# Optimization experiments

Hardware: AMD Instinct MI355X
Metric: run time of the kernel (lower is better)

Reference implementation:

```python
import math
import jax, jax.numpy as jnp
import numpy as np

NUM_HEADS = 16

def _alibi_slopes(n):
    def pow2(n):
        start = 2 ** (-2 ** (-(math.log2(n) - 3)))
        return [start * start ** i for i in range(n)]
    if math.log2(n).is_integer():
        return pow2(n)
    c = 2 ** math.floor(math.log2(n))
    return pow2(c) + _alibi_slopes(2 * c)[0::2][: n - c]

def _alibi_bias(num_heads, L):
    pos = np.arange(L)
    rel = (pos[None, :] - pos[:, None]).astype(np.float32)  # [L, L]
    slopes = np.asarray(_alibi_slopes(num_heads), dtype=np.float32)[:, None, None]
    bias = slopes * rel[None, :, :]  # [H, L, L]
    causal = pos[None, :] <= pos[:, None]
    bias = np.where(causal[None, :, :], bias, -np.inf).astype(np.float32)
    return jnp.asarray(bias)[None]  # [1, H, L, L]

def setup_inputs() -> dict:
    key = jax.random.key(0)
    ks = jax.random.split(key, 4)
    B, L, D = 2, 2048, 1024
    x = jax.random.normal(ks[0], (B, L, D), dtype=jnp.float32)
    W_in = jax.random.normal(ks[1], (D, 3 * D), dtype=jnp.float32) * 0.02
    b_in = jnp.zeros((3 * D,), dtype=jnp.float32)
    W_out = jax.random.normal(ks[2], (D, D), dtype=jnp.float32) * 0.02
    b_out = jnp.zeros((D,), dtype=jnp.float32)
    return {"x": x, "W_in": W_in, "b_in": b_in, "W_out": W_out, "b_out": b_out}

def reference(x, W_in, b_in, W_out, b_out):
    B, L, D = x.shape
    H = NUM_HEADS
    Dh = D // H
    qkv = x @ W_in + b_in  # [B, L, 3D]
    q, k, v = jnp.split(qkv, 3, axis=-1)
    # [B, H, L, Dh]
    q = q.reshape(B, L, H, Dh).transpose(0, 2, 1, 3)
    k = k.reshape(B, L, H, Dh).transpose(0, 2, 1, 3)
    v = v.reshape(B, L, H, Dh).transpose(0, 2, 1, 3)
    attn = jnp.einsum("bhqd,bhkd->bhqk", q, k) * (1.0 / math.sqrt(Dh))
    attn = attn + _alibi_bias(H, L)  # ALiBi + causal mask (-inf above diag)
    p = jax.nn.softmax(attn, axis=-1)
    out = jnp.einsum("bhqk,bhkd->bhqd", p, v)
    out = out.transpose(0, 2, 1, 3).reshape(B, L, D)
    out = out @ W_out + b_out
    return out, k, v
```

## Files before the change

### kernel.cpp

```cpp
#include <hip/hip_runtime.h>
#include <math.h>

typedef __bf16 bf16x8 __attribute__((ext_vector_type(8)));
typedef float  f32x4  __attribute__((ext_vector_type(4)));
typedef unsigned short u16x4 __attribute__((ext_vector_type(4)));

#define BATCH  2
#define SEQ    2048
#define DMODEL 1024
#define NHEAD  16
#define DHEAD  64
#define MROWS  4096
#define N_QKV  3072
#define KDIM   1024
#define OUTSECT (MROWS*DMODEL)

#define LOG2E 1.44269504088896f
#define QSCALE (0.125f * LOG2E)

__device__ inline __bf16 f2bf(float f) {
    unsigned u = __builtin_bit_cast(unsigned, f);
    unsigned r = (u + 0x7fffu + ((u >> 16) & 1u)) >> 16;
    return __builtin_bit_cast(__bf16, (unsigned short)r);
}

__device__ inline void gload16(const void* g, void* l) {
    __builtin_amdgcn_global_load_lds(
        (const __attribute__((address_space(1))) void*)g,
        (__attribute__((address_space(3))) void*)l, 16, 0, 0);
}

__device__ inline float dpp_max16(float x) {
    int v, t;
    v = __builtin_bit_cast(int, x);
    t = __builtin_amdgcn_update_dpp(v, v, 0xB1, 0xF, 0xF, false);
    x = fmaxf(x, __builtin_bit_cast(float, t));
    v = __builtin_bit_cast(int, x);
    t = __builtin_amdgcn_update_dpp(v, v, 0x4E, 0xF, 0xF, false);
    x = fmaxf(x, __builtin_bit_cast(float, t));
    v = __builtin_bit_cast(int, x);
    t = __builtin_amdgcn_update_dpp(v, v, 0x128, 0xF, 0xF, false);
    x = fmaxf(x, __builtin_bit_cast(float, t));
    v = __builtin_bit_cast(int, x);
    t = __builtin_amdgcn_update_dpp(v, v, 0x140, 0xF, 0xF, false);
    x = fmaxf(x, __builtin_bit_cast(float, t));
    return x;
}
__device__ inline float dpp_sum16(float x) {
    int v, t;
    v = __builtin_bit_cast(int, x);
    t = __builtin_amdgcn_update_dpp(v, v, 0xB1, 0xF, 0xF, false);
    x += __builtin_bit_cast(float, t);
    v = __builtin_bit_cast(int, x);
    t = __builtin_amdgcn_update_dpp(v, v, 0x4E, 0xF, 0xF, false);
    x += __builtin_bit_cast(float, t);
    v = __builtin_bit_cast(int, x);
    t = __builtin_amdgcn_update_dpp(v, v, 0x128, 0xF, 0xF, false);
    x += __builtin_bit_cast(float, t);
    v = __builtin_bit_cast(int, x);
    t = __builtin_amdgcn_update_dpp(v, v, 0x140, 0xF, 0xF, false);
    x += __builtin_bit_cast(float, t);
    return x;
}


__global__ __launch_bounds__(256) void cvt_x_k(const float* __restrict__ x,
                                               __bf16* __restrict__ xb) {
    size_t i = (size_t)blockIdx.x * 256 + threadIdx.x;
    const float4* p = (const float4*)x + i * 2;
    float4 a = p[0], b = p[1];
    __bf16 o[8] = {f2bf(a.x), f2bf(a.y), f2bf(a.z), f2bf(a.w),
                   f2bf(b.x), f2bf(b.y), f2bf(b.z), f2bf(b.w)};
    *(bf16x8*)(xb + i * 8) = *(bf16x8*)o;
}

__global__ __launch_bounds__(256) void cvt_wt_k(const float* __restrict__ W,
                                                __bf16* __restrict__ Wt, int Nw) {
    __shared__ float t[64][65];
    const int k0 = blockIdx.y * 64, n0 = blockIdx.x * 64;
    const int tid = threadIdx.x;
    #pragma unroll
    for (int u = 0; u < 4; ++u) {
        int idx = u * 256 + tid;
        int r = idx >> 4, c4 = (idx & 15) << 2;
        float4 v = *(const float4*)&W[(size_t)(k0 + r) * Nw + n0 + c4];
        t[r][c4] = v.x; t[r][c4 + 1] = v.y; t[r][c4 + 2] = v.z; t[r][c4 + 3] = v.w;
    }
    __syncthreads();
    #pragma unroll
    for (int u = 0; u < 2; ++u) {
        int idx = u * 256 + tid;
        int n = idx >> 3, k8 = (idx & 7) << 3;
        __bf16 o[8];
        #pragma unroll
        for (int i = 0; i < 8; ++i) o[i] = f2bf(t[k8 + i][n]);
        *(bf16x8*)&Wt[(size_t)(n0 + n) * KDIM + k0 + k8] = *(bf16x8*)o;
    }
}

template<int MODE, int FI, int FJ>
__global__ __launch_bounds__(256) void gemm_bf(
    const __bf16* __restrict__ A, const __bf16* __restrict__ Bt,
    const float* __restrict__ bias,
    float* __restrict__ fo, float* __restrict__ kf, float* __restrict__ vf,
    __bf16* __restrict__ qb, __bf16* __restrict__ kb, __bf16* __restrict__ vb,
    int nbx)
{
    constexpr int BMt = FI * 32, BNt = FJ * 32;
    __shared__ __align__(16) __bf16 As[BMt * 64];
    __shared__ __align__(16) __bf16 Bs[BNt * 64];

    const int tid = threadIdx.x, wid = tid >> 6, lane = tid & 63;
    const int l16 = lane & 15, lq = lane >> 4;
    const int wm = wid >> 1, wn = wid & 1;

    const int nwg = gridDim.x;
    const int bid = blockIdx.x;
    const int swz = (bid & 7) * (nwg >> 3) + (bid >> 3);
    const int m0 = (swz / nbx) * BMt;
    const int n0 = (swz % nbx) * BNt;

    const int lr8 = lane >> 3;
    const int colE = ((lane & 7) ^ lr8) << 3;

    f32x4 acc[FI][FJ];
    #pragma unroll
    for (int i = 0; i < FI; ++i)
        #pragma unroll
        for (int j = 0; j < FJ; ++j)
            acc[i][j] = f32x4{0.f, 0.f, 0.f, 0.f};

    for (int k0 = 0; k0 < KDIM; k0 += 64) {
        __syncthreads();
        #pragma unroll
        for (int c = wid; c < FI * 4 + FJ * 4; c += 4) {
            const bool isA = (c < FI * 4);
            const int ch = isA ? c : c - FI * 4;
            const int row = ch * 8 + lr8;
            const __bf16* src = isA ? (A  + (size_t)(m0 + row) * KDIM + k0 + colE)
                                    : (Bt + (size_t)(n0 + row) * KDIM + k0 + colE);
            gload16(src, (isA ? As : Bs) + ch * 512);
        }
        __syncthreads();
        #pragma unroll
        for (int kk = 0; kk < 2; ++kk) {
            bf16x8 af[FI], bfg[FJ];
            #pragma unroll
            for (int i = 0; i < FI; ++i) {
                int r = wm * (FI * 16) + i * 16 + l16;
                af[i] = *(const bf16x8*)&As[r * 64 + ((kk * 32 + lq * 8) ^ ((r & 7) << 3))];
            }
            #pragma unroll
            for (int j = 0; j < FJ; ++j) {
                int r = wn * (FJ * 16) + j * 16 + l16;
                bfg[j] = *(const bf16x8*)&Bs[r * 64 + ((kk * 32 + lq * 8) ^ ((r & 7) << 3))];
            }
            #pragma unroll
            for (int i = 0; i < FI; ++i)
                #pragma unroll
                for (int j = 0; j < FJ; ++j)
                    acc[i][j] = __builtin_amdgcn_mfma_f32_16x16x32_bf16(af[i], bfg[j], acc[i][j], 0, 0, 0);
        }
    }

    #pragma unroll
    for (int i = 0; i < FI; ++i) {
        #pragma unroll
        for (int j = 0; j < FJ; ++j) {
            const int col  = n0 + wn * (FJ * 16) + j * 16 + l16;
            const int rowb = m0 + wm * (FI * 16) + i * 16 + lq * 4;
            float v[4];
            #pragma unroll
            for (int r = 0; r < 4; ++r) v[r] = acc[i][j][r] + bias[col];
            if (MODE == 1) {
                #pragma unroll
                for (int r = 0; r < 4; ++r)
                    fo[(size_t)(rowb + r) * DMODEL + col] = v[r];
            } else {
                const int which = col >> 10, rem = col & 1023;
                const int h = rem >> 6, dh = rem & 63;
                const int bb = rowb >> 11, ll = rowb & 2047;
                const size_t lidx = ((size_t)(bb * NHEAD + h) * SEQ + ll) * DHEAD + dh;
                if (which == 0) {
                    #pragma unroll
                    for (int r = 0; r < 4; ++r)
                        qb[lidx + (size_t)r * DHEAD] = f2bf(v[r] * QSCALE);
                } else if (which == 1) {
                    #pragma unroll
                    for (int r = 0; r < 4; ++r) {
                        kf[lidx + (size_t)r * DHEAD] = v[r];
                        kb[lidx + (size_t)r * DHEAD] = f2bf(v[r]);
                    }
                } else {
                    u16x4 pk;
                    #pragma unroll
                    for (int r = 0; r < 4; ++r) {
                        vf[lidx + (size_t)r * DHEAD] = v[r];
                        pk[r] = __builtin_bit_cast(unsigned short, f2bf(v[r]));
                    }
                    *(u16x4*)&vb[((size_t)(bb * NHEAD + h) * DHEAD + dh) * SEQ + ll] = pk;
                }
            }
        }
    }
}

__global__ __launch_bounds__(256) void attn_k(
    const __bf16* __restrict__ Qb, const __bf16* __restrict__ Kb,
    const __bf16* __restrict__ Vb, __bf16* __restrict__ Ob)
{
    __shared__ __align__(16) __bf16 Qs[64 * 64];
    __shared__ __align__(16) __bf16 Ks[2][64 * 64];
    __shared__ __align__(16) __bf16 Vs[2][64 * 64];
    __shared__ __align__(16) __bf16 Ps[4 * 16 * 64];

    const int tid = threadIdx.x, wid = tid >> 6, lane = tid & 63;
    const int l16 = lane & 15, lq = lane >> 4;

    const int bid = blockIdx.x;
    const int t   = bid >> 3;
    const int qt  = 31 - (t >> 2);
    const int bh  = (bid & 7) * 4 + (t & 3);
    const int h = bh & 15, bb = bh >> 4;
    const int q0 = qt * 64;
    const size_t kvbase = (size_t)bh * SEQ * DHEAD;
    const float slope2 = exp2f(-0.5f * (float)(h + 1)) * LOG2E;
    const int qr0 = wid * 16;
    const int lr8 = lane >> 3;
    const int colE = ((lane & 7) ^ lr8) << 3;

    #pragma unroll
    for (int u = 0; u < 2; ++u) {
        int ch = u * 4 + wid;
        int row = ch * 8 + lr8;
        gload16(Qb + kvbase + (size_t)(q0 + row) * DHEAD + colE, Qs + ch * 512);
    }
    #pragma unroll
    for (int u = 0; u < 2; ++u) {
        int ch = u * 4 + wid;
        int row = ch * 8 + lr8;
        gload16(Kb + kvbase + (size_t)row * DHEAD + colE, Ks[0] + ch * 512);
        gload16(Vb + kvbase + (size_t)row * SEQ  + colE, Vs[0] + ch * 512);
    }
    __syncthreads();

    float ct[4][4];
    #pragma unroll
    for (int r = 0; r < 4; ++r) {
        const int qi = q0 + qr0 + lq * 4 + r;
        #pragma unroll
        for (int nf = 0; nf < 4; ++nf)
            ct[r][nf] = slope2 * (float)(nf * 16 + l16 - qi);
    }
    const float dtj = slope2 * 64.f;

    float mrow[4], lrow[4];
    f32x4 accO[4];
    #pragma unroll
    for (int r = 0; r < 4; ++r) { mrow[r] = -1e30f; lrow[r] = 0.f; }
    #pragma unroll
    for (int j = 0; j < 4; ++j) accO[j] = f32x4{0.f, 0.f, 0.f, 0.f};

    int cur = 0;
    for (int jt = 0; jt <= qt; ++jt) {
        if (jt < qt) {
            const int jn = (jt + 1) * 64;
            #pragma unroll
            for (int u = 0; u < 2; ++u) {
                int ch = u * 4 + wid;
                int row = ch * 8 + lr8;
                gload16(Kb + kvbase + (size_t)(jn + row) * DHEAD + colE, Ks[cur ^ 1] + ch * 512);
                gload16(Vb + kvbase + (size_t)row * SEQ + jn + colE,     Vs[cur ^ 1] + ch * 512);
            }
        }

        f32x4 s[4];
        #pragma unroll
        for (int nf = 0; nf < 4; ++nf) {
            #pragma unroll
            for (int r = 0; r < 4; ++r) s[nf][r] = ct[r][nf];
        }
        if (jt == qt) {
            #pragma unroll
            for (int nf = 0; nf < 4; ++nf)
                #pragma unroll
                for (int r = 0; r < 4; ++r)
                    if (nf * 16 + l16 > qr0 + lq * 4 + r) s[nf][r] = -3e38f;
        }

        const int qrow = qr0 + l16;
        bf16x8 aq0 = *(const bf16x8*)&Qs[qrow * 64 + ((lq * 8) ^ ((qrow & 7) << 3))];
        bf16x8 aq1 = *(const bf16x8*)&Qs[qrow * 64 + ((32 + lq * 8) ^ ((qrow & 7) << 3))];
        __builtin_amdgcn_s_setprio(1);
        #pragma unroll
        for (int nf = 0; nf < 4; ++nf) {
            int kr = nf * 16 + l16;
            bf16x8 bk0 = *(const bf16x8*)&Ks[cur][kr * 64 + ((lq * 8) ^ ((kr & 7) << 3))];
            bf16x8 bk1 = *(const bf16x8*)&Ks[cur][kr * 64 + ((32 + lq * 8) ^ ((kr & 7) << 3))];
            s[nf] = __builtin_amdgcn_mfma_f32_16x16x32_bf16(aq0, bk0, s[nf], 0, 0, 0);
            s[nf] = __builtin_amdgcn_mfma_f32_16x16x32_bf16(aq1, bk1, s[nf], 0, 0, 0);
        }
        __builtin_amdgcn_s_setprio(0);

        #pragma unroll
        for (int r = 0; r < 4; ++r) {
            float rm = fmaxf(fmaxf(s[0][r], s[1][r]), fmaxf(s[2][r], s[3][r]));
            rm = dpp_max16(rm);
            float mnew = fmaxf(mrow[r], rm);
            float p0 = __builtin_amdgcn_exp2f(s[0][r] - mnew);
            float p1 = __builtin_amdgcn_exp2f(s[1][r] - mnew);
            float p2 = __builtin_amdgcn_exp2f(s[2][r] - mnew);
            float p3 = __builtin_amdgcn_exp2f(s[3][r] - mnew);
            const int prow = lq * 4 + r;
            const int pb = wid * 1024 + prow * 64;
            const int px = (prow & 7) << 3;
            Ps[pb + ((l16     ) ^ px)] = (__bf16)p0;
            Ps[pb + ((l16 + 16) ^ px)] = (__bf16)p1;
            Ps[pb + ((l16 + 32) ^ px)] = (__bf16)p2;
            Ps[pb + ((l16 + 48) ^ px)] = (__bf16)p3;
            float rsum = dpp_sum16((p0 + p1) + (p2 + p3));
            float scale = __builtin_amdgcn_exp2f(mrow[r] - mnew);
            lrow[r] = lrow[r] * scale + rsum;
            mrow[r] = mnew;
            #pragma unroll
            for (int nf = 0; nf < 4; ++nf) accO[nf][r] *= scale;
        }
        #pragma unroll
        for (int r = 0; r < 4; ++r)
            #pragma unroll
            for (int nf = 0; nf < 4; ++nf) ct[r][nf] += dtj;

        bf16x8 ap0 = *(const bf16x8*)&Ps[wid * 1024 + l16 * 64 + ((lq * 8) ^ ((l16 & 7) << 3))];
        bf16x8 ap1 = *(const bf16x8*)&Ps[wid * 1024 + l16 * 64 + ((32 + lq * 8) ^ ((l16 & 7) << 3))];
        __builtin_amdgcn_s_setprio(1);
        #pragma unroll
        for (int nf = 0; nf < 4; ++nf) {
            int vr = nf * 16 + l16;
            bf16x8 bv0 = *(const bf16x8*)&Vs[cur][vr * 64 + ((lq * 8) ^ ((vr & 7) << 3))];
            bf16x8 bv1 = *(const bf16x8*)&Vs[cur][vr * 64 + ((32 + lq * 8) ^ ((vr & 7) << 3))];
            accO[nf] = __builtin_amdgcn_mfma_f32_16x16x32_bf16(ap0, bv0, accO[nf], 0, 0, 0);
            accO[nf] = __builtin_amdgcn_mfma_f32_16x16x32_bf16(ap1, bv1, accO[nf], 0, 0, 0);
        }
        __builtin_amdgcn_s_setprio(0);

        __syncthreads();
        cur ^= 1;
    }

    #pragma unroll
    for (int r = 0; r < 4; ++r) {
        const float inv = __builtin_amdgcn_rcpf(lrow[r]);
        const int qi = q0 + qr0 + lq * 4 + r;
        #pragma unroll
        for (int nf = 0; nf < 4; ++nf) {
            int dh = nf * 16 + l16;
            Ob[(size_t)(bb * SEQ + qi) * DMODEL + h * DHEAD + dh] = (__bf16)(accO[nf][r] * inv);
        }
    }
}

extern "C" void kernel_launch(void* const* d_in, const int* in_sizes, int n_in,
                              void* d_out, int out_size, void* d_ws, size_t ws_size,
                              hipStream_t stream) {
    const float* x     = (const float*)d_in[0];
    const float* W_in  = (const float*)d_in[1];
    const float* b_in  = (const float*)d_in[2];
    const float* W_out = (const float*)d_in[3];
    const float* b_out = (const float*)d_in[4];

    float* out = (float*)d_out;
    float* kf  = out + (size_t)OUTSECT;
    float* vf  = out + 2 * (size_t)OUTSECT;

    __bf16* qb = (__bf16*)d_out;
    __bf16* xb = (__bf16*)d_out + (size_t)OUTSECT;

    __bf16* ob  = (__bf16*)d_ws;
    __bf16* kb  = ob + (size_t)OUTSECT;
    __bf16* vb  = kb + (size_t)OUTSECT;
    __bf16* wti = vb + (size_t)OUTSECT;
    __bf16* wto = wti + (size_t)N_QKV * KDIM;

    cvt_x_k <<<2048, 256, 0, stream>>>(x, xb);
    cvt_wt_k<<<dim3(48, 16), 256, 0, stream>>>(W_in,  wti, N_QKV);
    cvt_wt_k<<<dim3(16, 16), 256, 0, stream>>>(W_out, wto, DMODEL);

    gemm_bf<0, 4, 4><<<768, 256, 0, stream>>>(xb, wti, b_in,
        nullptr, kf, vf, qb, kb, vb, N_QKV / 128);

    attn_k<<<1024, 256, 0, stream>>>(qb, kb, vb, ob);

    gemm_bf<1, 2, 4><<<512, 256, 0, stream>>>(ob, wto, b_out,
        out, nullptr, nullptr, nullptr, nullptr, nullptr, DMODEL / 128);
}
```

Before: 203.9 us.

## Merge conversion kernels, add lazy softmax rescaling, retile output GEMM

Folds the three fp32-to-bf16 conversion launches into one kernel that dispatches on block index, cutting launch overhead. In attention, the online-softmax rescale of the accumulators and row sums now runs only when some row max grows by more than 8 in log2 units; a wave-wide vote decides this, so most tiles skip the rescale. The ALiBi bias offset is now computed from the tile index rather than accumulated every iteration. The output GEMM switches from 2x4 to 4x4 tiling with half as many blocks. Lazy rescaling lets exponentials reach up to 2^8 before rescaling, which is fine in fp32 but adds a divergent branch.

Result: faster. 199.9 us (-2.0%).

```diff
diff --git a/kernel.cpp b/kernel.cpp
--- a/kernel.cpp
+++ b/kernel.cpp
@@ -63,22 +63,27 @@
     return x;
 }
 
-
-__global__ __launch_bounds__(256) void cvt_x_k(const float* __restrict__ x,
-                                               __bf16* __restrict__ xb) {
-    size_t i = (size_t)blockIdx.x * 256 + threadIdx.x;
-    const float4* p = (const float4*)x + i * 2;
-    float4 a = p[0], b = p[1];
-    __bf16 o[8] = {f2bf(a.x), f2bf(a.y), f2bf(a.z), f2bf(a.w),
-                   f2bf(b.x), f2bf(b.y), f2bf(b.z), f2bf(b.w)};
-    *(bf16x8*)(xb + i * 8) = *(bf16x8*)o;
-}
-
-__global__ __launch_bounds__(256) void cvt_wt_k(const float* __restrict__ W,
-                                                __bf16* __restrict__ Wt, int Nw) {
+__global__ __launch_bounds__(256) void cvt_all_k(
+    const float* __restrict__ x, __bf16* __restrict__ xb,
+    const float* __restrict__ W_in, __bf16* __restrict__ wti,
+    const float* __restrict__ W_out, __bf16* __restrict__ wto)
+{
     __shared__ float t[64][65];
-    const int k0 = blockIdx.y * 64, n0 = blockIdx.x * 64;
+    const int b = blockIdx.x;
     const int tid = threadIdx.x;
+    if (b < 2048) {
+        size_t i = (size_t)b * 256 + tid;
+        const float4* p = (const float4*)x + i * 2;
+        float4 a = p[0], c = p[1];
+        __bf16 o[8] = {f2bf(a.x), f2bf(a.y), f2bf(a.z), f2bf(a.w),
+                       f2bf(c.x), f2bf(c.y), f2bf(c.z), f2bf(c.w)};
+        *(bf16x8*)(xb + i * 8) = *(bf16x8*)o;
+        return;
+    }
+    const float* W;  __bf16* Wt;  int Nw, bx, by;
+    if (b < 2816) { int c = b - 2048; W = W_in;  Wt = wti; Nw = N_QKV;  bx = c % 48; by = c / 48; }
+    else          { int c = b - 2816; W = W_out; Wt = wto; Nw = DMODEL; bx = c % 16; by = c / 16; }
+    const int k0 = by * 64, n0 = bx * 64;
     #pragma unroll
     for (int u = 0; u < 4; ++u) {
         int idx = u * 256 + tid;
@@ -274,11 +279,12 @@
             }
         }
 
+        const float tb = dtj * (float)jt;
         f32x4 s[4];
         #pragma unroll
         for (int nf = 0; nf < 4; ++nf) {
             #pragma unroll
-            for (int r = 0; r < 4; ++r) s[nf][r] = ct[r][nf];
+            for (int r = 0; r < 4; ++r) s[nf][r] = ct[r][nf] + tb;
         }
         if (jt == qt) {
             #pragma unroll
@@ -302,15 +308,29 @@
         }
         __builtin_amdgcn_s_setprio(0);
 
+        float rm[4];
+        #pragma unroll
+        for (int r = 0; r < 4; ++r)
+            rm[r] = dpp_max16(fmaxf(fmaxf(s[0][r], s[1][r]), fmaxf(s[2][r], s[3][r])));
+        bool need = (rm[0] > mrow[0] + 8.f) || (rm[1] > mrow[1] + 8.f) ||
+                    (rm[2] > mrow[2] + 8.f) || (rm[3] > mrow[3] + 8.f);
+        if (__any(need)) {
+            #pragma unroll
+            for (int r = 0; r < 4; ++r) {
+                float mnew = fmaxf(mrow[r], rm[r]);
+                float scale = __builtin_amdgcn_exp2f(mrow[r] - mnew);
+                lrow[r] *= scale;
+                mrow[r] = mnew;
+                #pragma unroll
+                for (int nf = 0; nf < 4; ++nf) accO[nf][r] *= scale;
+            }
+        }
         #pragma unroll
         for (int r = 0; r < 4; ++r) {
-            float rm = fmaxf(fmaxf(s[0][r], s[1][r]), fmaxf(s[2][r], s[3][r]));
-            rm = dpp_max16(rm);
-            float mnew = fmaxf(mrow[r], rm);
-            float p0 = __builtin_amdgcn_exp2f(s[0][r] - mnew);
-            float p1 = __builtin_amdgcn_exp2f(s[1][r] - mnew);
-            float p2 = __builtin_amdgcn_exp2f(s[2][r] - mnew);
-            float p3 = __builtin_amdgcn_exp2f(s[3][r] - mnew);
+            float p0 = __builtin_amdgcn_exp2f(s[0][r] - mrow[r]);
+            float p1 = __builtin_amdgcn_exp2f(s[1][r] - mrow[r]);
+            float p2 = __builtin_amdgcn_exp2f(s[2][r] - mrow[r]);
+            float p3 = __builtin_amdgcn_exp2f(s[3][r] - mrow[r]);
             const int prow = lq * 4 + r;
             const int pb = wid * 1024 + prow * 64;
             const int px = (prow & 7) << 3;
@@ -318,17 +338,8 @@
             Ps[pb + ((l16 + 16) ^ px)] = (__bf16)p1;
             Ps[pb + ((l16 + 32) ^ px)] = (__bf16)p2;
             Ps[pb + ((l16 + 48) ^ px)] = (__bf16)p3;
-            float rsum = dpp_sum16((p0 + p1) + (p2 + p3));
-            float scale = __builtin_amdgcn_exp2f(mrow[r] - mnew);
-            lrow[r] = lrow[r] * scale + rsum;
-            mrow[r] = mnew;
-            #pragma unroll
-            for (int nf = 0; nf < 4; ++nf) accO[nf][r] *= scale;
-        }
-        #pragma unroll
-        for (int r = 0; r < 4; ++r)
-            #pragma unroll
-            for (int nf = 0; nf < 4; ++nf) ct[r][nf] += dtj;
+            lrow[r] += dpp_sum16((p0 + p1) + (p2 + p3));
+        }
 
         bf16x8 ap0 = *(const bf16x8*)&Ps[wid * 1024 + l16 * 64 + ((lq * 8) ^ ((l16 & 7) << 3))];
         bf16x8 ap1 = *(const bf16x8*)&Ps[wid * 1024 + l16 * 64 + ((32 + lq * 8) ^ ((l16 & 7) << 3))];
@@ -381,15 +392,13 @@
     __bf16* wti = vb + (size_t)OUTSECT;
     __bf16* wto = wti + (size_t)N_QKV * KDIM;
 
-    cvt_x_k <<<2048, 256, 0, stream>>>(x, xb);
-    cvt_wt_k<<<dim3(48, 16), 256, 0, stream>>>(W_in,  wti, N_QKV);
-    cvt_wt_k<<<dim3(16, 16), 256, 0, stream>>>(W_out, wto, DMODEL);
+    cvt_all_k<<<3072, 256, 0, stream>>>(x, xb, W_in, wti, W_out, wto);
 
     gemm_bf<0, 4, 4><<<768, 256, 0, stream>>>(xb, wti, b_in,
         nullptr, kf, vf, qb, kb, vb, N_QKV / 128);
 
     attn_k<<<1024, 256, 0, stream>>>(qb, kb, vb, ob);
 
-    gemm_bf<1, 2, 4><<<512, 256, 0, stream>>>(ob, wto, b_out,
+    gemm_bf<1, 4, 4><<<256, 256, 0, stream>>>(ob, wto, b_out,
         out, nullptr, nullptr, nullptr, nullptr, nullptr, DMODEL / 128);
 }
```
